# Kernel tuning notes

Hardware: AMD Instinct MI355X
Metric: run time of the kernel (lower is better)

The kernel has to match this reference:

```python
import jax, jax.numpy as jnp
import numpy as np

DIM = 2048
N_HEADS = 32
N_KV_HEADS = 8
HEAD_DIM = 64
REPEATS = N_HEADS // N_KV_HEADS
SCALE = HEAD_DIM ** -0.5
L = 2048
B = 1


def rotary_matrix(context_len, d):
    # Dense (L, d, d) RoPE rotation matrix, exactly as get_rotary_matrix1.
    pos = jnp.arange(1, context_len + 1, dtype=jnp.float32)[:, None]
    i = jnp.arange(d // 2)
    theta = 10000.0 ** (-2.0 * i.astype(jnp.float32) / d)
    m_theta = pos * theta  # (L, d/2)
    cos_v, sin_v = jnp.cos(m_theta), jnp.sin(m_theta)
    R = jnp.zeros((context_len, d, d), dtype=jnp.float32)
    R = R.at[:, 2 * i, 2 * i].set(cos_v)
    R = R.at[:, 2 * i, 2 * i + 1].set(-sin_v)
    R = R.at[:, 2 * i + 1, 2 * i].set(sin_v)
    R = R.at[:, 2 * i + 1, 2 * i + 1].set(cos_v)
    return R


def causal_mask(context_len):
    idx = jnp.arange(context_len)
    return (idx[:, None] < idx[None, :]).astype(jnp.float32) * -1e9


def setup_inputs() -> dict:
    key = jax.random.key(0)
    ks = jax.random.split(key, 5)
    x = jax.random.normal(ks[0], (B, L, DIM), dtype=jnp.float32)
    mask = causal_mask(L)
    wq_w = jax.random.normal(ks[1], (N_HEADS * HEAD_DIM, DIM), dtype=jnp.float32) * 0.02
    wk_w = jax.random.normal(ks[2], (N_KV_HEADS * HEAD_DIM, DIM), dtype=jnp.float32) * 0.02
    wv_w = jax.random.normal(ks[3], (N_KV_HEADS * HEAD_DIM, DIM), dtype=jnp.float32) * 0.02
    wo_w = jax.random.normal(ks[4], (DIM, N_HEADS * HEAD_DIM), dtype=jnp.float32) * 0.02
    return {"x": x, "mask": mask, "wq_w": wq_w, "wk_w": wk_w, "wv_w": wv_w, "wo_w": wo_w}


def reference(x, mask, wq_w, wk_w, wv_w, wo_w):
    Bx, Lx, D = x.shape
    # projections (torch Linear: y = x @ W.T)
    q = jnp.einsum('bld,od->blo', x, wq_w).reshape(Bx, Lx, N_HEADS, HEAD_DIM).transpose(0, 2, 1, 3)
    k = jnp.einsum('bld,od->blo', x, wk_w).reshape(Bx, Lx, N_KV_HEADS, HEAD_DIM).transpose(0, 2, 1, 3)
    v = jnp.einsum('bld,od->blo', x, wv_w).reshape(Bx, Lx, N_KV_HEADS, HEAD_DIM).transpose(0, 2, 1, 3)
    # GQA repeat of kv heads (interleaved, matching concat-unsqueeze-reshape)
    k = jnp.repeat(k, REPEATS, axis=1)
    v = jnp.repeat(v, REPEATS, axis=1)
    # dense-matrix RoPE on q and (repeated) k
    R = rotary_matrix(Lx, HEAD_DIM)
    q = jnp.einsum('bhlj,lij->bhli', q, R)
    k = jnp.einsum('bhlj,lij->bhli', k, R)
    scores = jnp.einsum('bhld,bhmd->bhlm', q, k) * SCALE + mask
    attn = jax.nn.softmax(scores.astype(jnp.float32), axis=-1)
    out = jnp.einsum('bhlm,bhmd->bhld', attn, v)
    out = out.transpose(0, 2, 1, 3).reshape(Bx, Lx, N_HEADS * HEAD_DIM)
    out = jnp.einsum('blo,do->bld', out, wo_w)
    return out, k, v
```

## Files before the change

kernel.cpp:

```cpp
#include <hip/hip_runtime.h>

typedef __bf16 bf16;
typedef __bf16 bf16x8 __attribute__((ext_vector_type(8)));
typedef float floatx4 __attribute__((ext_vector_type(4)));
typedef float floatx16 __attribute__((ext_vector_type(16)));
typedef unsigned int uint;

#define MFMA16(a, b, c) __builtin_amdgcn_mfma_f32_16x16x32_bf16((a), (b), (c), 0, 0, 0)
#define MFMA32(a, b, c) __builtin_amdgcn_mfma_f32_32x32x16_bf16((a), (b), (c), 0, 0, 0)

__device__ __forceinline__ void gl2lds16(const bf16* g, bf16* l) {
  __builtin_amdgcn_global_load_lds(
      (const __attribute__((address_space(1))) void*)g,
      (__attribute__((address_space(3))) void*)l, 16, 0, 0);
}
__device__ __forceinline__ void wait_vm0() { __builtin_amdgcn_s_waitcnt(0x0f70); }

__device__ __forceinline__ void cvt8(const float* __restrict__ s,
                                     bf16* __restrict__ d, int i8) {
  const float4 a = ((const float4*)s)[i8 * 2];
  const float4 b = ((const float4*)s)[i8 * 2 + 1];
  bf16x8 o;
  o[0] = (bf16)a.x; o[1] = (bf16)a.y; o[2] = (bf16)a.z; o[3] = (bf16)a.w;
  o[4] = (bf16)b.x; o[5] = (bf16)b.y; o[6] = (bf16)b.z; o[7] = (bf16)b.w;
  *(bf16x8*)(d + i8 * 8) = o;
}

__global__ __launch_bounds__(256) void convert_kernel(
    const float* __restrict__ x, const float* __restrict__ wq,
    const float* __restrict__ wk, const float* __restrict__ wv,
    const float* __restrict__ wo, bf16* __restrict__ xb,
    bf16* __restrict__ wqb, bf16* __restrict__ wkb, bf16* __restrict__ wvb,
    bf16* __restrict__ wob) {
  const int g = blockIdx.x * 256 + threadIdx.x;
  if (g < 524288) cvt8(x, xb, g);
  else if (g < 1048576) cvt8(wq, wqb, g - 524288);
  else if (g < 1179648) cvt8(wk, wkb, g - 1048576);
  else if (g < 1310720) cvt8(wv, wvb, g - 1179648);
  else cvt8(wo, wob, g - 1310720);
}

template <typename OutT>
__device__ __forceinline__ void gemm_tile_body32(
    const bf16* __restrict__ A, int lda,
    const bf16* __restrict__ B, int ldb,
    OutT* __restrict__ C, int ldc, int K,
    bf16* As, bf16* Bs) {
  const int t = threadIdx.x;
  const int w = t >> 6, lane = t & 63;
  const int l15 = lane & 15, qd = lane >> 4;
  const int wr = w >> 1, wc = w & 1;

  floatx4 acc[4][4];
#pragma unroll
  for (int i = 0; i < 4; ++i)
#pragma unroll
    for (int j = 0; j < 4; ++j) acc[i][j] = (floatx4){0.f, 0.f, 0.f, 0.f};

  const int mt0 = w, mt1 = w + 4;
  const int kseg = qd * 8;
  const bf16* ga0 = A + (mt0 * 16 + l15) * lda + kseg;
  const bf16* ga1 = A + (mt1 * 16 + l15) * lda + kseg;
  const bf16* gb0 = B + (mt0 * 16 + l15) * ldb + kseg;
  const bf16* gb1 = B + (mt1 * 16 + l15) * ldb + kseg;
  bf16* lA0 = As + mt0 * 512 + lane * 8;
  bf16* lA1 = As + mt1 * 512 + lane * 8;
  bf16* lB0 = Bs + mt0 * 512 + lane * 8;
  bf16* lB1 = Bs + mt1 * 512 + lane * 8;

  for (int k0 = 0; k0 < K; k0 += 32) {
    gl2lds16(ga0 + k0, lA0);
    gl2lds16(ga1 + k0, lA1);
    gl2lds16(gb0 + k0, lB0);
    gl2lds16(gb1 + k0, lB1);
    wait_vm0();
    __syncthreads();

    bf16x8 a[4], b[4];
#pragma unroll
    for (int i = 0; i < 4; ++i)
      a[i] = *(const bf16x8*)(As + (wr * 4 + i) * 512 + lane * 8);
#pragma unroll
    for (int j = 0; j < 4; ++j)
      b[j] = *(const bf16x8*)(Bs + (wc * 4 + j) * 512 + lane * 8);
#pragma unroll
    for (int i = 0; i < 4; ++i)
#pragma unroll
      for (int j = 0; j < 4; ++j) acc[i][j] = MFMA16(a[i], b[j], acc[i][j]);
    __syncthreads();
  }

#pragma unroll
  for (int i = 0; i < 4; ++i)
#pragma unroll
    for (int j = 0; j < 4; ++j) {
      const int row = wr * 64 + i * 16 + qd * 4;
      const int col = wc * 64 + j * 16 + l15;
#pragma unroll
      for (int r = 0; r < 4; ++r)
        C[(row + r) * ldc + col] = (OutT)acc[i][j][r];
    }
}

template <typename OutT>
__device__ __forceinline__ void gemm_tile_body64(
    const bf16* __restrict__ A, int lda,
    const bf16* __restrict__ B, int ldb,
    OutT* __restrict__ C, int ldc, int K,
    bf16* S) {
  const int t = threadIdx.x;
  const int w = t >> 6, lane = t & 63;
  const int l15 = lane & 15, qd = lane >> 4;
  const int wr = w >> 1, wc = w & 1;

  floatx4 acc[2][4];
#pragma unroll
  for (int i = 0; i < 2; ++i)
#pragma unroll
    for (int j = 0; j < 4; ++j) acc[i][j] = (floatx4){0.f, 0.f, 0.f, 0.f};

  const bf16* gb[6];
  int lo[6];
#pragma unroll
  for (int i = 0; i < 6; ++i) {
    const int u = w + 4 * i;
    lo[i] = u * 512 + lane * 8;
    if (u < 8) {
      gb[i] = A + ((u >> 1) * 16 + l15) * lda + (u & 1) * 32 + qd * 8;
    } else {
      const int v = u - 8;
      gb[i] = B + ((v >> 1) * 16 + l15) * ldb + (v & 1) * 32 + qd * 8;
    }
  }

#define STG64(kt_, buf_)                                            \
  {                                                                 \
    bf16* d_ = S + (buf_) * 12288;                                  \
    _Pragma("unroll")                                               \
    for (int i_ = 0; i_ < 6; ++i_)                                  \
      gl2lds16(gb[i_] + (kt_) * 64, d_ + lo[i_]);                   \
  }

  const int NT = K >> 6;
  STG64(0, 0);
  wait_vm0();
  __syncthreads();
  int cur = 0;
  for (int kt = 0; kt < NT; ++kt) {
    if (kt + 1 < NT) STG64(kt + 1, cur ^ 1);
    const bf16* Ab = S + cur * 12288;
    const bf16* Bb = Ab + 4096;
    bf16x8 a[2][2], b[4][2];
#pragma unroll
    for (int i = 0; i < 2; ++i)
#pragma unroll
      for (int kk = 0; kk < 2; ++kk)
        a[i][kk] =
            *(const bf16x8*)(Ab + ((wr * 2 + i) * 2 + kk) * 512 + lane * 8);
#pragma unroll
    for (int j = 0; j < 4; ++j)
#pragma unroll
      for (int kk = 0; kk < 2; ++kk)
        b[j][kk] =
            *(const bf16x8*)(Bb + ((wc * 4 + j) * 2 + kk) * 512 + lane * 8);
#pragma unroll
    for (int kk = 0; kk < 2; ++kk)
#pragma unroll
      for (int i = 0; i < 2; ++i)
#pragma unroll
        for (int j = 0; j < 4; ++j)
          acc[i][j] = MFMA16(a[i][kk], b[j][kk], acc[i][j]);
    wait_vm0();
    __builtin_amdgcn_sched_barrier(0);
    __builtin_amdgcn_s_barrier();
    __builtin_amdgcn_sched_barrier(0);
    cur ^= 1;
  }
#undef STG64

#pragma unroll
  for (int i = 0; i < 2; ++i)
#pragma unroll
    for (int j = 0; j < 4; ++j) {
      const int row = wr * 32 + i * 16 + qd * 4;
      const int col = wc * 64 + j * 16 + l15;
#pragma unroll
      for (int r = 0; r < 4; ++r)
        C[(row + r) * ldc + col] = (OutT)acc[i][j][r];
    }
}

__global__ __launch_bounds__(256) void gemm_qkv(
    const bf16* __restrict__ x, const bf16* __restrict__ wq,
    const bf16* __restrict__ wk, const bf16* __restrict__ wv,
    float* __restrict__ P) {
  __shared__ bf16 As[4096], Bs[4096];
  const int m0 = blockIdx.y * 128;
  const int nb = blockIdx.x;
  const int s = blockIdx.z;
  const bf16* B;
  if (nb < 16) B = wq + nb * 128 * 2048;
  else if (nb < 20) B = wk + (nb - 16) * 128 * 2048;
  else B = wv + (nb - 20) * 128 * 2048;
  float* C = P + s * 6291456 + m0 * 3072 + nb * 128;
  gemm_tile_body32<float>(x + m0 * 2048 + s * 1024, 2048, B + s * 1024, 2048,
                          C, 3072, 1024, As, Bs);
}

__global__ __launch_bounds__(256) void combine_qkv(
    const float* __restrict__ P, bf16* __restrict__ Qws,
    bf16* __restrict__ Kws, bf16* __restrict__ Vws) {
  const int g = blockIdx.x * 256 + threadIdx.x;
  const int base = g * 8;
  const int row = base / 3072;
  const int col = base - row * 3072;
  const float4 a0 = *(const float4*)(P + base);
  const float4 a1 = *(const float4*)(P + base + 4);
  const float4 b0 = *(const float4*)(P + 6291456 + base);
  const float4 b1 = *(const float4*)(P + 6291456 + base + 4);
  bf16x8 o;
  o[0] = (bf16)(a0.x + b0.x); o[1] = (bf16)(a0.y + b0.y);
  o[2] = (bf16)(a0.z + b0.z); o[3] = (bf16)(a0.w + b0.w);
  o[4] = (bf16)(a1.x + b1.x); o[5] = (bf16)(a1.y + b1.y);
  o[6] = (bf16)(a1.z + b1.z); o[7] = (bf16)(a1.w + b1.w);
  bf16* dst;
  if (col < 2048) dst = Qws + row * 2048 + col;
  else if (col < 2560) dst = Kws + row * 512 + (col - 2048);
  else dst = Vws + row * 512 + (col - 2560);
  *(bf16x8*)dst = o;
}

__global__ __launch_bounds__(256) void gemm_o(
    const bf16* __restrict__ Ows, const bf16* __restrict__ wo,
    float* __restrict__ out) {
  __shared__ bf16 S[24576];
  const int m0 = blockIdx.y * 64, n0 = blockIdx.x * 128;
  gemm_tile_body64<float>(Ows + m0 * 2048, 2048, wo + n0 * 2048, 2048,
                          out + m0 * 2048 + n0, 2048, 2048, S);
}

__global__ __launch_bounds__(256) void rope_repeat_kernel(
    bf16* __restrict__ Qws, bf16* __restrict__ Kws, bf16* __restrict__ Kh,
    const bf16* __restrict__ Vws, bf16* __restrict__ Vt,
    float* __restrict__ kout, float* __restrict__ vout) {
  const int gid = blockIdx.x * 256 + threadIdx.x;
  const float NEG_LOG2_10000_D32 = -0.4152410118609203f;
  if (gid < 2097152) {
    const int l = gid >> 10, pr = gid & 1023, a = pr & 31;
    bf16* p = Qws + l * 2048 + pr * 2;
    const float x0 = (float)p[0], x1 = (float)p[1];
    const float ang = (float)(l + 1) * exp2f(NEG_LOG2_10000_D32 * (float)a);
    float s, c;
    __sincosf(ang, &s, &c);
    p[0] = (bf16)(c * x0 - s * x1);
    p[1] = (bf16)(s * x0 + c * x1);
  } else if (gid < 2097152 + 524288) {
    const int g = gid - 2097152;
    const int l = g >> 8, pr = g & 255, a = pr & 31, kvh = pr >> 5;
    bf16* p = Kws + l * 512 + pr * 2;
    const float x0 = (float)p[0], x1 = (float)p[1];
    const float ang = (float)(l + 1) * exp2f(NEG_LOG2_10000_D32 * (float)a);
    float s, c;
    __sincosf(ang, &s, &c);
    const float y0 = c * x0 - s * x1;
    const float y1 = s * x0 + c * x1;
    p[0] = (bf16)y0;
    p[1] = (bf16)y1;
    bf16* kp = Kh + (kvh * 2048 + l) * 64 + a * 2;
    kp[0] = (bf16)y0;
    kp[1] = (bf16)y1;
#pragma unroll
    for (int rep = 0; rep < 4; ++rep) {
      float* o = kout + (((kvh * 4 + rep) * 2048 + l) * 64 + a * 2);
      o[0] = y0;
      o[1] = y1;
    }
  } else if (gid < 2097152 + 524288 + 131072) {
    const int c = gid - (2097152 + 524288);
    const int l = c >> 6, seg = c & 63, kvh = seg >> 3;
    const bf16x8 v = *(const bf16x8*)(Vws + l * 512 + seg * 8);
    float4 f0, f1;
    f0.x = (float)v[0]; f0.y = (float)v[1]; f0.z = (float)v[2]; f0.w = (float)v[3];
    f1.x = (float)v[4]; f1.y = (float)v[5]; f1.z = (float)v[6]; f1.w = (float)v[7];
#pragma unroll
    for (int rep = 0; rep < 4; ++rep) {
      float* o = vout + (((kvh * 4 + rep) * 2048 + l) * 64 + (seg & 7) * 8);
      *(float4*)o = f0;
      *(float4*)(o + 4) = f1;
    }
  } else {
    const int c = gid - (2097152 + 524288 + 131072);
    const int kvh = c >> 14, r2 = c & 16383, dseg = r2 >> 11, l = r2 & 2047;
    const int d0 = dseg * 8;
    const bf16x8 v = *(const bf16x8*)(Vws + l * 512 + kvh * 64 + d0);
#pragma unroll
    for (int jj = 0; jj < 8; ++jj)
      Vt[kvh * 131072 + (d0 + jj) * 2048 + l] = v[jj];
  }
}

__global__ __launch_bounds__(256) void flash_kernel(
    const bf16* __restrict__ Qws, const bf16* __restrict__ Kh,
    const bf16* __restrict__ Vt, bf16* __restrict__ Ows,
    float* __restrict__ Opart, float* __restrict__ ML) {
  __shared__ bf16 KVs[2][2][4096];
  __shared__ bf16 Osh[128 * 66];

  const int h = blockIdx.y;
  const int bx = blockIdx.x;
  int qt, seg, kts, kte;
  if (bx < 8) {
    qt = bx; seg = -1; kts = 0; kte = 2 * qt + 2;
  } else {
    const int i = bx - 8;
    qt = 8 + (i >> 1);
    seg = i & 1;
    const int half = qt + 1;
    kts = seg * half;
    kte = kts + half;
  }
  const int kh = h >> 2;
  const int q0 = qt * 128;
  const int t = threadIdx.x, w = t >> 6, lane = t & 63;
  const int l31 = lane & 31, hf = lane >> 5;
  const int qw = q0 + w * 32;

  bf16x8 qf[4];
  {
    const bf16* qrow = Qws + (qw + l31) * 2048 + h * 64 + hf * 8;
#pragma unroll
    for (int c = 0; c < 4; ++c) qf[c] = *(const bf16x8*)(qrow + c * 16);
  }

  floatx16 o[2] = {};
  float mrun = -3e38f, lrun = 0.f;

  const int s0 = w, s1 = w + 4;
  const bf16* gK0 = Kh + kh * 131072 + ((s0 >> 2) * 32 + l31) * 64 + (s0 & 3) * 16 + hf * 8;
  const bf16* gK1 = Kh + kh * 131072 + ((s1 >> 2) * 32 + l31) * 64 + (s1 & 3) * 16 + hf * 8;
  const bf16* gV0 = Vt + kh * 131072 + ((s0 >> 2) * 32 + l31) * 2048 + (s0 & 3) * 16 + hf * 8;
  const bf16* gV1 = Vt + kh * 131072 + ((s1 >> 2) * 32 + l31) * 2048 + (s1 & 3) * 16 + hf * 8;

  {
    const int nb = kts & 1;
    gl2lds16(gK0 + kts * 4096, &KVs[nb][0][s0 * 512 + lane * 8]);
    gl2lds16(gK1 + kts * 4096, &KVs[nb][0][s1 * 512 + lane * 8]);
    gl2lds16(gV0 + kts * 64, &KVs[nb][1][s0 * 512 + lane * 8]);
    gl2lds16(gV1 + kts * 64, &KVs[nb][1][s1 * 512 + lane * 8]);
  }

  const float C = 0.1803368801f;
  for (int kt = kts; kt < kte; ++kt) {
    wait_vm0();
    __syncthreads();
    if (kt + 1 < kte) {
      const int nb = (kt + 1) & 1;
      const int koff = (kt + 1) * 4096, voff = (kt + 1) * 64;
      gl2lds16(gK0 + koff, &KVs[nb][0][s0 * 512 + lane * 8]);
      gl2lds16(gK1 + koff, &KVs[nb][0][s1 * 512 + lane * 8]);
      gl2lds16(gV0 + voff, &KVs[nb][1][s0 * 512 + lane * 8]);
      gl2lds16(gV1 + voff, &KVs[nb][1][s1 * 512 + lane * 8]);
    }
    const int kt64 = kt * 64;
    if (kt64 > qw + 31) continue;
    const bf16* Kb = &KVs[kt & 1][0][0];
    const bf16* Vb = &KVs[kt & 1][1][0];

    floatx16 st[2];
    __builtin_amdgcn_s_setprio(1);
#pragma unroll
    for (int tt = 0; tt < 2; ++tt) {
      floatx16 z = {};
#pragma unroll
      for (int c = 0; c < 4; ++c) {
        const bf16x8 kf = *(const bf16x8*)(Kb + (tt * 4 + c) * 512 + lane * 8);
        z = MFMA32(kf, qf[c], z);
      }
      st[tt] = z;
    }
    __builtin_amdgcn_s_setprio(0);
    if (kt64 + 64 > qw) {
      const int myq = qw + l31;
#pragma unroll
      for (int tt = 0; tt < 2; ++tt)
#pragma unroll
        for (int r = 0; r < 16; ++r) {
          const int key = kt64 + tt * 32 + (r & 3) + 8 * (r >> 2) + 4 * hf;
          if (key > myq) st[tt][r] = -1e30f;
        }
    }
    float ma = -3e38f, mb = -3e38f, mc = -3e38f, md = -3e38f;
#pragma unroll
    for (int tt = 0; tt < 2; ++tt)
#pragma unroll
      for (int r = 0; r < 16; r += 4) {
        ma = fmaxf(ma, st[tt][r + 0]);
        mb = fmaxf(mb, st[tt][r + 1]);
        mc = fmaxf(mc, st[tt][r + 2]);
        md = fmaxf(md, st[tt][r + 3]);
      }
    float mx = fmaxf(fmaxf(ma, mb), fmaxf(mc, md));
    mx = fmaxf(mx, __shfl_xor(mx, 32));
    const bool defer = __all((mx - mrun) * C <= 8.f);
    if (!defer) {
      const float mn = fmaxf(mrun, mx);
      const float al = __builtin_amdgcn_exp2f((mrun - mn) * C);
      lrun *= al;
#pragma unroll
      for (int n = 0; n < 2; ++n)
#pragma unroll
        for (int r = 0; r < 16; ++r) o[n][r] *= al;
      mrun = mn;
    }
    float ra = 0.f, rb = 0.f, rc = 0.f, rd = 0.f;
#pragma unroll
    for (int tt = 0; tt < 2; ++tt)
#pragma unroll
      for (int r = 0; r < 16; r += 4) {
        const float p0 = __builtin_amdgcn_exp2f((st[tt][r + 0] - mrun) * C);
        const float p1 = __builtin_amdgcn_exp2f((st[tt][r + 1] - mrun) * C);
        const float p2 = __builtin_amdgcn_exp2f((st[tt][r + 2] - mrun) * C);
        const float p3 = __builtin_amdgcn_exp2f((st[tt][r + 3] - mrun) * C);
        st[tt][r + 0] = p0; ra += p0;
        st[tt][r + 1] = p1; rb += p1;
        st[tt][r + 2] = p2; rc += p2;
        st[tt][r + 3] = p3; rd += p3;
      }
    float rs = (ra + rb) + (rc + rd);
    rs += __shfl_xor(rs, 32);
    lrun += rs;

    uint pk[2][4][2];
#pragma unroll
    for (int tt = 0; tt < 2; ++tt)
#pragma unroll
      for (int g = 0; g < 4; ++g)
#pragma unroll
        for (int p = 0; p < 2; ++p) {
          union { bf16 h2[2]; uint u; } cv;
          cv.h2[0] = (bf16)st[tt][4 * g + 2 * p];
          cv.h2[1] = (bf16)st[tt][4 * g + 2 * p + 1];
          pk[tt][g][p] = cv.u;
        }
    uint own_[2][2][2], rv[2][2][2];
#pragma unroll
    for (int tt = 0; tt < 2; ++tt)
#pragma unroll
      for (int gam = 0; gam < 2; ++gam)
#pragma unroll
        for (int p = 0; p < 2; ++p) {
          own_[tt][gam][p] = hf ? pk[tt][2 * gam + 1][p] : pk[tt][2 * gam][p];
          const uint snd = hf ? pk[tt][2 * gam][p] : pk[tt][2 * gam + 1][p];
          rv[tt][gam][p] = (uint)__shfl_xor((int)snd, 32);
        }
    __builtin_amdgcn_s_setprio(1);
#pragma unroll
    for (int c = 0; c < 4; ++c) {
      const int tt = c >> 1, gam = c & 1;
      union { uint u[4]; bf16x8 v; } pf;
      pf.u[0] = hf ? rv[tt][gam][0] : own_[tt][gam][0];
      pf.u[1] = hf ? rv[tt][gam][1] : own_[tt][gam][1];
      pf.u[2] = hf ? own_[tt][gam][0] : rv[tt][gam][0];
      pf.u[3] = hf ? own_[tt][gam][1] : rv[tt][gam][1];
#pragma unroll
      for (int n = 0; n < 2; ++n)
        o[n] = MFMA32(*(const bf16x8*)(Vb + (n * 4 + c) * 512 + lane * 8),
                      pf.v, o[n]);
    }
    __builtin_amdgcn_s_setprio(0);
  }

  if (seg < 0) {
    const float inv = 1.f / lrun;
#pragma unroll
    for (int n = 0; n < 2; ++n)
#pragma unroll
      for (int r = 0; r < 16; ++r) {
        const int dl = n * 32 + (r & 3) + 8 * (r >> 2) + 4 * hf;
        Osh[(w * 32 + l31) * 66 + dl] = (bf16)(o[n][r] * inv);
      }
    __syncthreads();
#pragma unroll
    for (int i = 0; i < 4; ++i) {
      const int row = (t >> 3) + i * 32;
      const int col = (t & 7) * 8;
      const bf16x8 vv = *(const bf16x8*)&Osh[row * 66 + col];
      *(bf16x8*)&Ows[(q0 + row) * 2048 + h * 64 + col] = vv;
    }
  } else {
    const int idx = (h * 8 + (qt - 8)) * 2 + seg;
    float* Op = Opart + idx * 8192;
#pragma unroll
    for (int n = 0; n < 2; ++n)
#pragma unroll
      for (int r = 0; r < 16; ++r) {
        const int dl = n * 32 + (r & 3) + 8 * (r >> 2) + 4 * hf;
        Op[dl * 128 + w * 32 + l31] = o[n][r];
      }
    if (hf == 0) {
      ML[idx * 256 + w * 32 + l31] = mrun;
      ML[idx * 256 + 128 + w * 32 + l31] = lrun;
    }
  }
}

__global__ __launch_bounds__(256) void combine_kernel(
    const float* __restrict__ Opart, const float* __restrict__ ML,
    bf16* __restrict__ Ows) {
  __shared__ bf16 Osh[128 * 66];
  const int b = blockIdx.x;
  const int h = b >> 3, qt = (b & 7) + 8;
  const int q0 = qt * 128;
  const int t = threadIdx.x;
  const int row = t & 127, dh = t >> 7;
  const int i0 = (h * 8 + (qt - 8)) * 2;
  const float C = 0.1803368801f;
  const float m0 = ML[i0 * 256 + row], l0 = ML[i0 * 256 + 128 + row];
  const float m1 = ML[(i0 + 1) * 256 + row], l1 = ML[(i0 + 1) * 256 + 128 + row];
  const float m = fmaxf(m0, m1);
  const float w0 = __builtin_amdgcn_exp2f((m0 - m) * C);
  const float w1 = __builtin_amdgcn_exp2f((m1 - m) * C);
  const float inv = 1.f / (l0 * w0 + l1 * w1);
  const float* P0 = Opart + i0 * 8192;
  const float* P1 = Opart + (i0 + 1) * 8192;
#pragma unroll
  for (int j = 0; j < 32; ++j) {
    const int d = dh * 32 + j;
    const float v = (P0[d * 128 + row] * w0 + P1[d * 128 + row] * w1) * inv;
    Osh[row * 66 + d] = (bf16)v;
  }
  __syncthreads();
#pragma unroll
  for (int i = 0; i < 4; ++i) {
    const int r2 = (t >> 3) + i * 32;
    const int col = (t & 7) * 8;
    const bf16x8 vv = *(const bf16x8*)&Osh[r2 * 66 + col];
    *(bf16x8*)&Ows[(q0 + r2) * 2048 + h * 64 + col] = vv;
  }
}

extern "C" void kernel_launch(void* const* d_in, const int* in_sizes, int n_in,
                              void* d_out, int out_size, void* d_ws,
                              size_t ws_size, hipStream_t stream) {
  const float* x = (const float*)d_in[0];
  const float* wq = (const float*)d_in[2];
  const float* wk = (const float*)d_in[3];
  const float* wv = (const float*)d_in[4];
  const float* wo = (const float*)d_in[5];

  float* out = (float*)d_out;
  float* kout = out + 4194304;
  float* vout = out + 8388608;

  bf16* ws = (bf16*)d_ws;
  bf16* xb = ws;
  bf16* wqb = xb + 4194304;
  bf16* wkb = wqb + 4194304;
  bf16* wvb = wkb + 1048576;
  bf16* wob = wvb + 1048576;
  bf16* Qws = wob + 4194304;
  bf16* Kws = Qws + 4194304;
  bf16* Vws = Kws + 1048576;
  bf16* Vt = Vws + 1048576;
  bf16* Ows = Vt + 1048576;
  bf16* Kh = Ows + 4194304;
  float* Pqkv = out;
  float* Opart = out;
  float* MLf = (float*)Kws;

  convert_kernel<<<dim3(7168), dim3(256), 0, stream>>>(x, wq, wk, wv, wo, xb,
                                                       wqb, wkb, wvb, wob);
  gemm_qkv<<<dim3(24, 16, 2), dim3(256), 0, stream>>>(xb, wqb, wkb, wvb, Pqkv);
  combine_qkv<<<dim3(3072), dim3(256), 0, stream>>>(Pqkv, Qws, Kws, Vws);
  rope_repeat_kernel<<<dim3(11264), dim3(256), 0, stream>>>(Qws, Kws, Kh, Vws,
                                                            Vt, kout, vout);
  flash_kernel<<<dim3(24, 32), dim3(256), 0, stream>>>(Qws, Kh, Vt, Ows, Opart,
                                                       MLf);
  combine_kernel<<<dim3(256), dim3(256), 0, stream>>>(Opart, MLf, Ows);
  gemm_o<<<dim3(16, 32), dim3(256), 0, stream>>>(Ows, wob, out);
}
```

Measured before the change: 307.5 us.

## Drop split-K in QKV GEMM, write bf16 directly, add block swizzle

The QKV projection GEMM now runs the full K=2048 reduction in one pass and writes bf16 results straight into the Q, K and V workspaces. This removes the fp32 partial-sum buffers and the separate combine kernel. The grid halves to 384 blocks, which may lower occupancy on a GPU with many CUs. A block-index swizzle is also added to both gemm_qkv and gemm_o to group blocks for better L2 reuse.

```diff
diff --git a/kernel.cpp b/kernel.cpp
--- a/kernel.cpp
+++ b/kernel.cpp
@@ -193,48 +193,39 @@
 __global__ __launch_bounds__(256) void gemm_qkv(
     const bf16* __restrict__ x, const bf16* __restrict__ wq,
     const bf16* __restrict__ wk, const bf16* __restrict__ wv,
-    float* __restrict__ P) {
+    bf16* __restrict__ Qws, bf16* __restrict__ Kws, bf16* __restrict__ Vws) {
   __shared__ bf16 As[4096], Bs[4096];
-  const int m0 = blockIdx.y * 128;
-  const int nb = blockIdx.x;
-  const int s = blockIdx.z;
+  const int bid = blockIdx.y * 24 + blockIdx.x;
+  const int swz = (bid & 7) * 48 + (bid >> 3);
+  const int nb = swz % 24;
+  const int m0 = (swz / 24) * 128;
   const bf16* B;
-  if (nb < 16) B = wq + nb * 128 * 2048;
-  else if (nb < 20) B = wk + (nb - 16) * 128 * 2048;
-  else B = wv + (nb - 20) * 128 * 2048;
-  float* C = P + s * 6291456 + m0 * 3072 + nb * 128;
-  gemm_tile_body32<float>(x + m0 * 2048 + s * 1024, 2048, B + s * 1024, 2048,
-                          C, 3072, 1024, As, Bs);
-}
-
-__global__ __launch_bounds__(256) void combine_qkv(
-    const float* __restrict__ P, bf16* __restrict__ Qws,
-    bf16* __restrict__ Kws, bf16* __restrict__ Vws) {
-  const int g = blockIdx.x * 256 + threadIdx.x;
-  const int base = g * 8;
-  const int row = base / 3072;
-  const int col = base - row * 3072;
-  const float4 a0 = *(const float4*)(P + base);
-  const float4 a1 = *(const float4*)(P + base + 4);
-  const float4 b0 = *(const float4*)(P + 6291456 + base);
-  const float4 b1 = *(const float4*)(P + 6291456 + base + 4);
-  bf16x8 o;
-  o[0] = (bf16)(a0.x + b0.x); o[1] = (bf16)(a0.y + b0.y);
-  o[2] = (bf16)(a0.z + b0.z); o[3] = (bf16)(a0.w + b0.w);
-  o[4] = (bf16)(a1.x + b1.x); o[5] = (bf16)(a1.y + b1.y);
-  o[6] = (bf16)(a1.z + b1.z); o[7] = (bf16)(a1.w + b1.w);
-  bf16* dst;
-  if (col < 2048) dst = Qws + row * 2048 + col;
-  else if (col < 2560) dst = Kws + row * 512 + (col - 2048);
-  else dst = Vws + row * 512 + (col - 2560);
-  *(bf16x8*)dst = o;
+  bf16* C;
+  int ldc;
+  if (nb < 16) {
+    B = wq + nb * 128 * 2048;
+    C = Qws + m0 * 2048 + nb * 128;
+    ldc = 2048;
+  } else if (nb < 20) {
+    B = wk + (nb - 16) * 128 * 2048;
+    C = Kws + m0 * 512 + (nb - 16) * 128;
+    ldc = 512;
+  } else {
+    B = wv + (nb - 20) * 128 * 2048;
+    C = Vws + m0 * 512 + (nb - 20) * 128;
+    ldc = 512;
+  }
+  gemm_tile_body32<bf16>(x + m0 * 2048, 2048, B, 2048, C, ldc, 2048, As, Bs);
 }
 
 __global__ __launch_bounds__(256) void gemm_o(
     const bf16* __restrict__ Ows, const bf16* __restrict__ wo,
     float* __restrict__ out) {
   __shared__ bf16 S[24576];
-  const int m0 = blockIdx.y * 64, n0 = blockIdx.x * 128;
+  const int bid = blockIdx.y * 16 + blockIdx.x;
+  const int swz = (bid & 7) * 64 + (bid >> 3);
+  const int n0 = (swz & 15) * 128;
+  const int m0 = (swz >> 4) * 64;
   gemm_tile_body64<float>(Ows + m0 * 2048, 2048, wo + n0 * 2048, 2048,
                           out + m0 * 2048 + n0, 2048, 2048, S);
 }
@@ -564,14 +555,13 @@
   bf16* Vt = Vws + 1048576;
   bf16* Ows = Vt + 1048576;
   bf16* Kh = Ows + 4194304;
-  float* Pqkv = out;
   float* Opart = out;
   float* MLf = (float*)Kws;
 
   convert_kernel<<<dim3(7168), dim3(256), 0, stream>>>(x, wq, wk, wv, wo, xb,
                                                        wqb, wkb, wvb, wob);
-  gemm_qkv<<<dim3(24, 16, 2), dim3(256), 0, stream>>>(xb, wqb, wkb, wvb, Pqkv);
-  combine_qkv<<<dim3(3072), dim3(256), 0, stream>>>(Pqkv, Qws, Kws, Vws);
+  gemm_qkv<<<dim3(24, 16), dim3(256), 0, stream>>>(xb, wqb, wkb, wvb, Qws, Kws,
+                                                   Vws);
   rope_repeat_kernel<<<dim3(11264), dim3(256), 0, stream>>>(Qws, Kws, Kh, Vws,
                                                             Vt, kout, vout);
   flash_kernel<<<dim3(24, 32), dim3(256), 0, stream>>>(Qws, Kh, Vt, Ows, Opart,
```

Result: faster. 289.0 us (-6.0%).
